# Kernel optimization log

Hardware: AMD Instinct MI355X
Metric: run time of the kernel (lower is better)

The kernel has to match this reference:

```python
import jax, jax.numpy as jnp
import numpy as np

N_NODES = 10000
N_EDGES = 320000
NUM_NEIGHBORS = 32.0
INV_SQRT3 = 1.0 / np.sqrt(3.0)  # component-normalized CG for 1o x 1o -> 0e


def setup_inputs() -> dict:
    key = jax.random.key(0)
    ks = jax.random.split(key, 16)
    f32 = jnp.float32
    return {
        "node_input": jax.random.normal(ks[0], (N_NODES, 160), f32),   # 64x0e | 32x1o
        "node_attr": jnp.ones((N_NODES, 1), f32),                       # 1x0e
        "edge_attr": jax.random.normal(ks[1], (N_EDGES, 4), f32),       # 1x0e | 1x1o (sph harm)
        "edge_scalar_attr": jax.random.normal(ks[2], (N_EDGES, 8), f32),# radial basis
        "Wsc0": jax.random.normal(ks[3], (64, 64), f32),
        "Wsc1": jax.random.normal(ks[4], (32, 32), f32),
        "Wl1_0": jax.random.normal(ks[5], (64, 64), f32),
        "Wl1_1": jax.random.normal(ks[6], (32, 32), f32),
        "Wfc1": jax.random.normal(ks[7], (8, 64), f32),
        "Wfc2": jax.random.normal(ks[8], (64, 64), f32),
        "Wfc3": jax.random.normal(ks[9], (64, 192), f32),  # -> tp.weight_numel
        "Wl2_s": jax.random.normal(ks[10], (96, 64), f32),
        "Wl2_v": jax.random.normal(ks[11], (96, 32), f32),
        "Wa": jax.random.normal(ks[12], (96, 1), f32),
        "edge_src": jax.random.randint(ks[13], (N_EDGES,), 0, N_NODES),
        "edge_dst": jax.random.randint(ks[14], (N_EDGES,), 0, N_NODES),
    }


def _fctp_scalar_attr(xs, xv, Ws, Wv, a):
    """FullyConnectedTensorProduct(irreps, '0e', irreps) with scalar node attr a.
    xs: [N, mul_s] scalars, xv: [N, mul_v, 3] vectors. Path-normalized by 1/sqrt(fan_in)."""
    out_s = (xs @ Ws) * (a / np.sqrt(xs.shape[1]))[:, None]
    out_v = jnp.einsum('nuc,uw->nwc', xv, Wv) * (a / np.sqrt(xv.shape[1]))[:, None, None]
    return out_s, out_v


def reference(node_input, node_attr, edge_attr, edge_scalar_attr,
              Wsc0, Wsc1, Wl1_0, Wl1_1, Wfc1, Wfc2, Wfc3, Wl2_s, Wl2_v, Wa,
              edge_src, edge_dst):
    N = node_input.shape[0]
    a = node_attr[:, 0]                              # [N] scalar attr
    xs = node_input[:, :64]                          # [N,64]  64x0e
    xv = node_input[:, 64:].reshape(N, 32, 3)        # [N,32,3] 32x1o

    # self connection: FCTp(input, attr, output)
    sc_s, sc_v = _fctp_scalar_attr(xs, xv, Wsc0, Wsc1, a)
    # lin1: FCTp(input, attr, input)
    f_s, f_v = _fctp_scalar_attr(xs, xv, Wl1_0, Wl1_1, a)

    # radial MLP -> tensor-product weights [E, 192]
    h = jax.nn.gelu(edge_scalar_attr @ Wfc1 / np.sqrt(8.0))
    h = jax.nn.gelu(h @ Wfc2 / np.sqrt(64.0))
    w = h @ Wfc3 / np.sqrt(64.0)
    w0, w1, w2, w3 = w[:, :64], w[:, 64:128], w[:, 128:160], w[:, 160:192]

    # gather source node features per edge
    gs = f_s[edge_src]                               # [E,64]
    gv = f_v[edge_src]                               # [E,32,3]
    y0 = edge_attr[:, 0]                             # [E]   0e
    y1 = edge_attr[:, 1:4]                           # [E,3] 1o

    # 'uvu' tensor product, irreps_mid (sorted) = 64x0e + 32x0e + 64x1o + 32x1o
    mid0 = w0 * gs * y0[:, None]                                        # 0e x 0e -> 0e
    mid1 = w3 * jnp.einsum('euc,ec->eu', gv, y1) * INV_SQRT3            # 1o x 1o -> 0e
    mid2 = (w1 * gs)[:, :, None] * y1[:, None, :]                       # 0e x 1o -> 1o
    mid3 = w2[:, :, None] * gv * y0[:, None, None]                      # 1o x 0e -> 1o

    # scatter-add to destination nodes, normalized by sqrt(num_neighbors)
    inv = 1.0 / np.sqrt(NUM_NEIGHBORS)
    seg = lambda x: jax.ops.segment_sum(x, edge_dst, num_segments=N) * inv
    ns0, ns1, nv2, nv3 = seg(mid0), seg(mid1), seg(mid2), seg(mid3)

    mid_s = jnp.concatenate([ns0, ns1], axis=1)      # [N,96] scalars of irreps_mid
    mid_v = jnp.concatenate([nv2, nv3], axis=1)      # [N,96,3] vectors of irreps_mid

    # lin2: FCTp(mid, attr, output), fan_in = 96 for both scalar and vector outputs
    out_s = (mid_s @ Wl2_s) * (a / np.sqrt(96.0))[:, None]
    out_v = jnp.einsum('nuc,uw->nwc', mid_v, Wl2_v) * (a / np.sqrt(96.0))[:, None, None]

    # alpha: FCTp(mid, attr, '0e'); self_con output_mask is all ones here
    alpha = (mid_s @ Wa) * (a / np.sqrt(96.0))[:, None]  # [N,1]

    res_s = sc_s + alpha * out_s
    res_v = sc_v + alpha[:, :, None] * out_v
    return jnp.concatenate([res_s, res_v.reshape(N, 96)], axis=1)  # [N,160]
```

## Files before the change

### kernel.cpp

```cpp
#include <hip/hip_runtime.h>

#define N_NODES 10000
#define N_EDGES 320000
#define INV3 0.5773502691896258f

typedef short short8 __attribute__((ext_vector_type(8)));
typedef float f32x4 __attribute__((ext_vector_type(4)));

__device__ __forceinline__ float gelu_f(float x) {
    float x3 = x * x * x;
    float e = __expf(-1.5957691216057308f * (x + 0.044715f * x3));
    return x * __builtin_amdgcn_rcpf(1.0f + e);
}

__device__ __forceinline__ unsigned short f2bf(float f) {
    unsigned u = __float_as_uint(f);
    unsigned r = (u + 0x7FFFu + ((u >> 16) & 1u)) >> 16;
    return (unsigned short)r;
}
__device__ __forceinline__ float bf2f(unsigned short u) {
    return __uint_as_float(((unsigned)u) << 16);
}
__device__ __forceinline__ unsigned cvtpk(float lo, float hi) {
    unsigned r;
    asm("v_cvt_pk_bf16_f32 %0, %1, %2" : "=v"(r) : "v"(lo), "v"(hi));
    return r;
}

__device__ __forceinline__ float rowsum16(float v) {
    v += __int_as_float(__builtin_amdgcn_update_dpp(0, __float_as_int(v), 0x118, 0xf, 0xf, true));
    v += __int_as_float(__builtin_amdgcn_update_dpp(0, __float_as_int(v), 0x114, 0xf, 0xf, true));
    v += __int_as_float(__builtin_amdgcn_update_dpp(0, __float_as_int(v), 0x112, 0xf, 0xf, true));
    v += __int_as_float(__builtin_amdgcn_update_dpp(0, __float_as_int(v), 0x111, 0xf, 0xf, true));
    return v;
}

__global__ __launch_bounds__(256) void pre_kernel(
    const int* __restrict__ edge_dst, int* __restrict__ deg,
    const float* __restrict__ Wfc1, const float* __restrict__ Wfc2,
    const float* __restrict__ Wfc3, uint4* __restrict__ fragbuf,
    const float* __restrict__ node_input, const float* __restrict__ node_attr,
    const float* __restrict__ Wl1_0, const float* __restrict__ Wl1_1,
    unsigned short* __restrict__ f_sb, unsigned short* __restrict__ f_vb,
    int* __restrict__ bcnt)
{
    const int b = blockIdx.x;
    if (b < 1250) {
        int e = b * 256 + threadIdx.x;
        if (e < N_EDGES) atomicAdd(&deg[edge_dst[e]], 1);
        return;
    }
    if (b < 1259) {
        if (b == 1250 && threadIdx.x < 64) bcnt[threadIdx.x] = 0;
        const int tile = (b - 1250) * 4 + (threadIdx.x >> 6);
        if (tile >= 36) return;
        const int l = threadIdx.x & 63;
        const int e = l & 15, g = l >> 4;
        unsigned p[4] = {0u, 0u, 0u, 0u};
        if (tile < 4) {
            if (g == 0) {
                #pragma unroll
                for (int j = 0; j < 8; ++j) {
                    unsigned short bb = f2bf(Wfc1[j * 64 + tile * 16 + e]);
                    p[j >> 1] |= (unsigned)bb << (16 * (j & 1));
                }
            }
        } else if (tile < 12) {
            int t2 = tile - 4; int mt = t2 >> 1, kt = t2 & 1;
            #pragma unroll
            for (int j = 0; j < 8; ++j) {
                unsigned short bb = f2bf(Wfc2[(kt * 32 + g * 8 + j) * 64 + mt * 16 + e]);
                p[j >> 1] |= (unsigned)bb << (16 * (j & 1));
            }
        } else {
            int t3 = tile - 12; int mt3 = t3 >> 1, kt = t3 & 1;
            #pragma unroll
            for (int j = 0; j < 8; ++j) {
                unsigned short bb = f2bf(Wfc3[(kt * 32 + g * 8 + j) * 192 + mt3 * 16 + e]);
                p[j >> 1] |= (unsigned)bb << (16 * (j & 1));
            }
        }
        uint4 v; v.x = p[0]; v.y = p[1]; v.z = p[2]; v.w = p[3];
        fragbuf[tile * 64 + l] = v;
        return;
    }
    const int wid = threadIdx.x >> 6;
    const int t = threadIdx.x & 63;
    const int n = (b - 1259) * 4 + wid;
    __shared__ float x[4][160];
    const float* row = node_input + (size_t)n * 160;
    for (int i = t; i < 160; i += 64) x[wid][i] = row[i];
    const float a = node_attr[n];

    float acc = 0.f;
    for (int k = 0; k < 64; ++k) acc += x[wid][k] * Wl1_0[k * 64 + t];
    f_sb[(size_t)n * 64 + t] = f2bf(acc * (a * 0.125f));

    const float sv = a * 0.17677669529663687f;
    for (int o = t; o < 96; o += 64) {
        int w = o / 3, c = o - w * 3;
        float av = 0.f;
        for (int u = 0; u < 32; ++u) av += x[wid][64 + u * 3 + c] * Wl1_1[u * 32 + w];
        f_vb[(size_t)n * 96 + o] = f2bf(av * sv);
    }
}

__global__ __launch_bounds__(256) void alloc_kernel(const int* __restrict__ deg,
                                                    int* __restrict__ gctr,
                                                    int* __restrict__ done,
                                                    int* __restrict__ rowptr,
                                                    int* __restrict__ cursor,
                                                    int* __restrict__ bcnt,
                                                    int* __restrict__ bcur) {
    const int tid = threadIdx.x;
    const int n = blockIdx.x * 256 + tid;
    const int d = (n < N_NODES) ? deg[n] : 0;

    __shared__ int part[256];
    __shared__ int blockbase;
    __shared__ int lb[64];
    __shared__ int islast;
    part[tid] = d;
    if (tid < 64) lb[tid] = 0;
    __syncthreads();
    for (int o = 1; o < 256; o <<= 1) {
        int v = (tid >= o) ? part[tid - o] : 0;
        __syncthreads();
        part[tid] += v;
        __syncthreads();
    }
    if (tid == 255) blockbase = atomicAdd(gctr, part[255]);
    __syncthreads();
    const int base = blockbase + part[tid] - d;
    if (n < N_NODES) {
        rowptr[n] = base;
        cursor[n] = base;
        int nt = (d + 15) >> 4; if (nt > 63) nt = 63;
        atomicAdd(&lb[nt], 1);
    }
    __syncthreads();
    if (tid < 64 && lb[tid]) {
        int ack = atomicAdd(&bcnt[tid], lb[tid]);
        asm volatile("" :: "v"(ack));
    }
    __syncthreads();
    if (tid == 0) islast = (atomicAdd(done, 1) == (int)gridDim.x - 1);
    __syncthreads();
    if (islast && tid == 0) {
        int run = 0;
        for (int i = 63; i >= 0; --i) { bcur[i] = run; run += atomicAdd(&bcnt[i], 0); }
    }
}

__global__ __launch_bounds__(256) void post_kernel(const int* __restrict__ dst,
                                                   const int* __restrict__ deg,
                                                   int* __restrict__ cursor,
                                                   int* __restrict__ elist,
                                                   int* __restrict__ bcur,
                                                   int* __restrict__ nodeperm) {
    const int b = blockIdx.x;
    if (b < 40) {
        const int tid = threadIdx.x;
        const int n = b * 256 + tid;
        __shared__ int lcnt[64], lbase[64];
        if (tid < 64) lcnt[tid] = 0;
        __syncthreads();
        int nt = 63, my = 0;
        if (n < N_NODES) {
            int d = deg[n];
            nt = (d + 15) >> 4; if (nt > 63) nt = 63;
            my = atomicAdd(&lcnt[nt], 1);
        }
        __syncthreads();
        if (tid < 64 && lcnt[tid]) lbase[tid] = atomicAdd(&bcur[tid], lcnt[tid]);
        __syncthreads();
        if (n < N_NODES) nodeperm[lbase[nt] + my] = n;
        return;
    }
    int e = (b - 40) * 256 + threadIdx.x;
    if (e < N_EDGES) {
        int p = atomicAdd(&cursor[dst[e]], 1);
        elist[p] = e;
    }
}

#define L3CHUNK(mt3_, d_) { \
    short8 a0_ = ((short8*)wfrag)[(12 + (mt3_) * 2 + 0) * 64 + l]; \
    short8 a1_ = ((short8*)wfrag)[(12 + (mt3_) * 2 + 1) * 64 + l]; \
    d_[0] = 0.f; d_[1] = 0.f; d_[2] = 0.f; d_[3] = 0.f; \
    d_ = __builtin_amdgcn_mfma_f32_16x16x32_bf16(a0_, bh0, d_, 0, 0, 0); \
    d_ = __builtin_amdgcn_mfma_f32_16x16x32_bf16(a1_, bh1, d_, 0, 0, 0); }

__global__ __launch_bounds__(256) __attribute__((amdgpu_waves_per_eu(2, 4)))
void fused_kernel(
    const float* __restrict__ edge_attr,
    const float* __restrict__ esa,
    const unsigned short* __restrict__ f_sb,
    const unsigned short* __restrict__ f_vb,
    const int* __restrict__ edge_src,
    const int* __restrict__ elist,
    const int* __restrict__ rowptr,
    const int* __restrict__ deg,
    const int* __restrict__ nodeperm,
    const float4* __restrict__ fragbuf,
    const float* __restrict__ node_input,
    const float* __restrict__ node_attr,
    const float* __restrict__ Wsc0,
    const float* __restrict__ Wsc1,
    const float* __restrict__ Wl2_s,
    const float* __restrict__ Wl2_v,
    const float* __restrict__ Wa,
    float* __restrict__ out)
{
    __shared__ __align__(16) char wfrag[36864];
    __shared__ __align__(16) char albuf[2 * 4096];
    __shared__ __align__(16) float xld[2][160];

    const int tid = threadIdx.x;
    const int l = tid & 63;
    const int wid = tid >> 6;
    const int q = wid & 1;
    const int ns = wid >> 1;

    {
        float4* w = (float4*)wfrag;
        #pragma unroll
        for (int i = 0; i < 9; ++i) w[tid + 256 * i] = fragbuf[tid + 256 * i];
    }

    const int n0 = nodeperm[blockIdx.x * 2 + 0];
    const int n1 = nodeperm[blockIdx.x * 2 + 1];
    const int n = ns ? n1 : n0;
    const int dn0 = deg[n0], dn1 = deg[n1];
    const int ntmax = ((dn0 > dn1 ? dn0 : dn1) + 15) >> 4;
    const int p0 = rowptr[n];
    const int p1 = p0 + (ns ? dn1 : dn0);
    const int p0c = p0 < N_EDGES ? p0 : N_EDGES - 1;

    if (q == 0)
        for (int i = l; i < 160; i += 64) xld[ns][i] = node_input[(size_t)n * 160 + i];

    __syncthreads();

    const int er = l & 15, gr = l >> 4;
    const int swz = (er & 7) << 4;
    char* h1b = albuf + ns * 4096;
    char* h2b = h1b + 2048;

    float acc0[2][4];
    float acc1[4];
    float acc2[2][4][3];
    float acc3[4][3];
    #pragma unroll
    for (int jj = 0; jj < 2; ++jj)
        #pragma unroll
        for (int r = 0; r < 4; ++r) {
            acc0[jj][r] = 0.f;
            acc2[jj][r][0] = 0.f; acc2[jj][r][1] = 0.f; acc2[jj][r][2] = 0.f;
        }
    #pragma unroll
    for (int r = 0; r < 4; ++r) {
        acc1[r] = 0.f;
        acc3[r][0] = 0.f; acc3[r][1] = 0.f; acc3[r][2] = 0.f;
    }

    float4 ea = {0.f, 0.f, 0.f, 0.f};
    int src = 0;
    uint4 bxu = {0u, 0u, 0u, 0u};
    if (ntmax > 0) {
        const int ci = p0 + er;
        const bool cv = ci < p1;
        const int ec = elist[cv ? ci : p0c];
        ea = ((const float4*)edge_attr)[ec];
        src = edge_src[ec];
        if (l < 16 && cv) {
            float4 xa = ((const float4*)esa)[(size_t)ec * 2 + 0];
            float4 xb = ((const float4*)esa)[(size_t)ec * 2 + 1];
            bxu.x = cvtpk(xa.x, xa.y);
            bxu.y = cvtpk(xa.z, xa.w);
            bxu.z = cvtpk(xb.x, xb.y);
            bxu.w = cvtpk(xb.z, xb.w);
        }
    }

    #pragma unroll 1
    for (int it = 0; it < ntmax; ++it) {
        const float y0 = ea.x, y1a = ea.y, y1b = ea.z, y1c = ea.w;
        union { uint4 u; short8 s; } bxc; bxc.u = bxu;
        const short8 bx = bxc.s;
        const int csrc = src;

        ushort4 gsu0 = *(const ushort4*)(f_sb + (size_t)csrc * 64 + (q * 2 + 0) * 16 + gr * 4);
        ushort4 gsu1 = *(const ushort4*)(f_sb + (size_t)csrc * 64 + (q * 2 + 1) * 16 + gr * 4);
        const unsigned short* gvp = f_vb + (size_t)csrc * 96 + (size_t)(q * 16 + gr * 4) * 3;
        ushort4 ga = *(const ushort4*)(gvp + 0);
        ushort4 gb = *(const ushort4*)(gvp + 4);
        ushort4 gc = *(const ushort4*)(gvp + 8);

        {
            const int np = p0 + (it + 1) * 16;
            const bool nv = (np + er) < p1;
            const int nec = elist[nv ? np + er : p0c];
            float4 nea = ((const float4*)edge_attr)[nec];
            int nsrc = edge_src[nec];
            uint4 nbxu = {0u, 0u, 0u, 0u};
            if (l < 16 && nv) {
                float4 xa = ((const float4*)esa)[(size_t)nec * 2 + 0];
                float4 xb = ((const float4*)esa)[(size_t)nec * 2 + 1];
                nbxu.x = cvtpk(xa.x, xa.y);
                nbxu.y = cvtpk(xa.z, xa.w);
                nbxu.z = cvtpk(xb.x, xb.y);
                nbxu.w = cvtpk(xb.z, xb.w);
            }
            ea = nea; src = nsrc; bxu = nbxu;
        }

        #pragma unroll
        for (int j = 0; j < 2; ++j) {
            const int mt = q * 2 + j;
            short8 aw = ((short8*)wfrag)[mt * 64 + l];
            f32x4 c = {0.f, 0.f, 0.f, 0.f};
            c = __builtin_amdgcn_mfma_f32_16x16x32_bf16(aw, bx, c, 0, 0, 0);
            unsigned pa = cvtpk(gelu_f(c[0] * 0.35355339059327373f),
                                gelu_f(c[1] * 0.35355339059327373f));
            unsigned pb = cvtpk(gelu_f(c[2] * 0.35355339059327373f),
                                gelu_f(c[3] * 0.35355339059327373f));
            uint2 pv; pv.x = pa; pv.y = pb;
            *(uint2*)(h1b + ((er * 128 + mt * 32 + gr * 8) ^ swz)) = pv;
        }
        __syncthreads();
        {
            short8 b0 = *(short8*)(h1b + ((er * 128 + 0  + gr * 16) ^ swz));
            short8 b1 = *(short8*)(h1b + ((er * 128 + 64 + gr * 16) ^ swz));
            #pragma unroll
            for (int j = 0; j < 2; ++j) {
                const int mt = q * 2 + j;
                short8 w2a = ((short8*)(wfrag + 4096))[(2 * mt + 0) * 64 + l];
                short8 w2b = ((short8*)(wfrag + 4096))[(2 * mt + 1) * 64 + l];
                f32x4 c = {0.f, 0.f, 0.f, 0.f};
                c = __builtin_amdgcn_mfma_f32_16x16x32_bf16(w2a, b0, c, 0, 0, 0);
                c = __builtin_amdgcn_mfma_f32_16x16x32_bf16(w2b, b1, c, 0, 0, 0);
                unsigned pa = cvtpk(gelu_f(c[0] * 0.125f), gelu_f(c[1] * 0.125f));
                unsigned pb = cvtpk(gelu_f(c[2] * 0.125f), gelu_f(c[3] * 0.125f));
                uint2 pv; pv.x = pa; pv.y = pb;
                *(uint2*)(h2b + ((er * 128 + mt * 32 + gr * 8) ^ swz)) = pv;
            }
        }
        __syncthreads();
        short8 bh0 = *(short8*)(h2b + ((er * 128 + 0  + gr * 16) ^ swz));
        short8 bh1 = *(short8*)(h2b + ((er * 128 + 64 + gr * 16) ^ swz));

        #pragma unroll
        for (int jj = 0; jj < 2; ++jj) {
            const int jg = q * 2 + jj;
            ushort4 gsu = jj ? gsu1 : gsu0;
            f32x4 gs4 = {bf2f(gsu.x), bf2f(gsu.y), bf2f(gsu.z), bf2f(gsu.w)};
            f32x4 dA; L3CHUNK(jg, dA);
            f32x4 dB; L3CHUNK(jg + 4, dB);
            #pragma unroll
            for (int r = 0; r < 4; ++r) {
                acc0[jj][r] += 0.125f * dA[r] * gs4[r] * y0;
                float t_ = 0.125f * dB[r] * gs4[r];
                acc2[jj][r][0] += t_ * y1a;
                acc2[jj][r][1] += t_ * y1b;
                acc2[jj][r][2] += t_ * y1c;
            }
        }
        {
            const int jv = q;
            float gv[12] = {bf2f(ga.x), bf2f(ga.y), bf2f(ga.z), bf2f(ga.w),
                            bf2f(gb.x), bf2f(gb.y), bf2f(gb.z), bf2f(gb.w),
                            bf2f(gc.x), bf2f(gc.y), bf2f(gc.z), bf2f(gc.w)};
            f32x4 dC; L3CHUNK(8 + jv, dC);
            f32x4 dD; L3CHUNK(10 + jv, dD);
            #pragma unroll
            for (int r = 0; r < 4; ++r) {
                float w2v = 0.125f * dC[r] * y0;
                acc3[r][0] += w2v * gv[r * 3 + 0];
                acc3[r][1] += w2v * gv[r * 3 + 1];
                acc3[r][2] += w2v * gv[r * 3 + 2];
                float dot = gv[r * 3 + 0] * y1a + gv[r * 3 + 1] * y1b + gv[r * 3 + 2] * y1c;
                acc1[r] += 0.125f * dD[r] * dot * INV3;
            }
        }
    }

    #pragma unroll
    for (int jj = 0; jj < 2; ++jj)
        #pragma unroll
        for (int r = 0; r < 4; ++r) {
            acc0[jj][r] = rowsum16(acc0[jj][r]);
            acc2[jj][r][0] = rowsum16(acc2[jj][r][0]);
            acc2[jj][r][1] = rowsum16(acc2[jj][r][1]);
            acc2[jj][r][2] = rowsum16(acc2[jj][r][2]);
        }
    #pragma unroll
    for (int r = 0; r < 4; ++r) {
        acc1[r] = rowsum16(acc1[r]);
        acc3[r][0] = rowsum16(acc3[r][0]);
        acc3[r][1] = rowsum16(acc3[r][1]);
        acc3[r][2] = rowsum16(acc3[r][2]);
    }

    __syncthreads();

    float* m = (float*)(albuf + ns * 4096);
    const float iN = 0.17677669529663687f;
    if (er == 15) {
        #pragma unroll
        for (int jj = 0; jj < 2; ++jj) {
            const int jg = q * 2 + jj;
            f32x4 v;
            v[0] = acc0[jj][0] * iN; v[1] = acc0[jj][1] * iN;
            v[2] = acc0[jj][2] * iN; v[3] = acc0[jj][3] * iN;
            *(f32x4*)(m + jg * 16 + gr * 4) = v;
        }
        {
            const int jv = q;
            f32x4 v;
            v[0] = acc1[0] * iN; v[1] = acc1[1] * iN;
            v[2] = acc1[2] * iN; v[3] = acc1[3] * iN;
            *(f32x4*)(m + 64 + jv * 16 + gr * 4) = v;
        }
        #pragma unroll
        for (int jj = 0; jj < 2; ++jj) {
            const int jg = q * 2 + jj;
            float t[12];
            #pragma unroll
            for (int r = 0; r < 4; ++r) {
                t[r * 3 + 0] = acc2[jj][r][0] * iN;
                t[r * 3 + 1] = acc2[jj][r][1] * iN;
                t[r * 3 + 2] = acc2[jj][r][2] * iN;
            }
            float* b = m + 96 + (jg * 16 + gr * 4) * 3;
            *(f32x4*)(b + 0) = (f32x4){t[0], t[1], t[2], t[3]};
            *(f32x4*)(b + 4) = (f32x4){t[4], t[5], t[6], t[7]};
            *(f32x4*)(b + 8) = (f32x4){t[8], t[9], t[10], t[11]};
        }
        {
            const int jv = q;
            float t[12];
            #pragma unroll
            for (int r = 0; r < 4; ++r) {
                t[r * 3 + 0] = acc3[r][0] * iN;
                t[r * 3 + 1] = acc3[r][1] * iN;
                t[r * 3 + 2] = acc3[r][2] * iN;
            }
            float* b = m + 288 + (jv * 16 + gr * 4) * 3;
            *(f32x4*)(b + 0) = (f32x4){t[0], t[1], t[2], t[3]};
            *(f32x4*)(b + 4) = (f32x4){t[4], t[5], t[6], t[7]};
            *(f32x4*)(b + 8) = (f32x4){t[8], t[9], t[10], t[11]};
        }
    }

    __syncthreads();

    const float a = node_attr[n];
    const float* x = xld[ns];
    const float s96 = a * 0.10206207261596575f;

    float alpha = 0.f;
    for (int i = 0; i < 96; ++i) alpha += m[i] * Wa[i];
    alpha *= s96;

    if (q == 0) {
        float outs = 0.f;
        for (int i = 0; i < 96; ++i) outs += m[i] * Wl2_s[i * 64 + l];
        outs *= s96;
        float scs = 0.f;
        for (int k = 0; k < 64; ++k) scs += x[k] * Wsc0[k * 64 + l];
        scs *= a * 0.125f;
        out[(size_t)n * 160 + l] = scs + alpha * outs;
    } else {
        const float sv = a * 0.17677669529663687f;
        for (int o = l; o < 96; o += 64) {
            int w = o / 3, c = o - w * 3;
            float ov = 0.f;
            for (int u = 0; u < 64; ++u) ov += m[96 + u * 3 + c] * Wl2_v[u * 32 + w];
            for (int u = 0; u < 32; ++u) ov += m[288 + u * 3 + c] * Wl2_v[(64 + u) * 32 + w];
            ov *= s96;
            float scv = 0.f;
            for (int u = 0; u < 32; ++u) scv += x[64 + u * 3 + c] * Wsc1[u * 32 + w];
            scv *= sv;
            out[(size_t)n * 160 + 64 + o] = scv + alpha * ov;
        }
    }
}

extern "C" void kernel_launch(void* const* d_in, const int* in_sizes, int n_in,
                              void* d_out, int out_size, void* d_ws, size_t ws_size,
                              hipStream_t stream) {
    const float* node_input = (const float*)d_in[0];
    const float* node_attr  = (const float*)d_in[1];
    const float* edge_attr  = (const float*)d_in[2];
    const float* esa        = (const float*)d_in[3];
    const float* Wsc0       = (const float*)d_in[4];
    const float* Wsc1       = (const float*)d_in[5];
    const float* Wl1_0      = (const float*)d_in[6];
    const float* Wl1_1      = (const float*)d_in[7];
    const float* Wfc1       = (const float*)d_in[8];
    const float* Wfc2       = (const float*)d_in[9];
    const float* Wfc3       = (const float*)d_in[10];
    const float* Wl2_s      = (const float*)d_in[11];
    const float* Wl2_v      = (const float*)d_in[12];
    const float* Wa         = (const float*)d_in[13];
    const int* edge_src     = (const int*)d_in[14];
    const int* edge_dst     = (const int*)d_in[15];
    float* out = (float*)d_out;

    float* ws  = (float*)d_ws;
    unsigned short* f_sb = (unsigned short*)ws;
    unsigned short* f_vb = (unsigned short*)(ws + 320000);
    uint4* fragbuf = (uint4*)(ws + 1600000);
    int* ibuf     = (int*)(ws + 1609216);
    int* deg      = ibuf;
    int* gctr     = ibuf + 10000;
    int* done     = ibuf + 10001;
    int* rowptr   = ibuf + 10016;
    int* cursor   = ibuf + 20032;
    int* elist    = ibuf + 30080;
    int* bcnt     = ibuf + 350080;
    int* bcur     = ibuf + 350144;
    int* nodeperm = ibuf + 350208;

    hipMemsetAsync(deg, 0, (size_t)(N_NODES + 2) * sizeof(int), stream);

    pre_kernel<<<3759, 256, 0, stream>>>(edge_dst, deg, Wfc1, Wfc2, Wfc3, fragbuf,
                                         node_input, node_attr, Wl1_0, Wl1_1, f_sb, f_vb, bcnt);
    alloc_kernel<<<(N_NODES + 255) / 256, 256, 0, stream>>>(deg, gctr, done, rowptr,
                                                            cursor, bcnt, bcur);
    post_kernel<<<40 + (N_EDGES + 255) / 256, 256, 0, stream>>>(edge_dst, deg, cursor,
                                                                elist, bcur, nodeperm);

    fused_kernel<<<N_NODES / 2, 256, 0, stream>>>(edge_attr, esa, f_sb, f_vb,
                                                  edge_src, elist, rowptr, deg, nodeperm,
                                                  (const float4*)fragbuf,
                                                  node_input, node_attr,
                                                  Wsc0, Wsc1, Wl2_s, Wl2_v, Wa,
                                                  out);
}
```

Baseline: 177.2 us.

## Process three nodes per block and two edge tiles per iteration

The fused kernel now runs 384 threads per block and handles three destination nodes instead of two. Each loop iteration now processes two 16-edge tiles with duplicated MFMA and GELU streams, which halves the number of block barriers per edge and adds more independent work to hide latency. The 0.125 scale of the last layer moves into the precomputed bf16 node features, so the inner loop does fewer multiplies. In exchange it uses more registers and LDS per block, and it takes the tile count from the first node only, which relies on the node permutation putting the highest-degree node first in each block.

```diff
diff --git a/kernel.cpp b/kernel.cpp
--- a/kernel.cpp
+++ b/kernel.cpp
@@ -94,14 +94,14 @@
 
     float acc = 0.f;
     for (int k = 0; k < 64; ++k) acc += x[wid][k] * Wl1_0[k * 64 + t];
-    f_sb[(size_t)n * 64 + t] = f2bf(acc * (a * 0.125f));
+    f_sb[(size_t)n * 64 + t] = f2bf(acc * (a * 0.125f) * 0.125f);
 
     const float sv = a * 0.17677669529663687f;
     for (int o = t; o < 96; o += 64) {
         int w = o / 3, c = o - w * 3;
         float av = 0.f;
         for (int u = 0; u < 32; ++u) av += x[wid][64 + u * 3 + c] * Wl1_1[u * 32 + w];
-        f_vb[(size_t)n * 96 + o] = f2bf(av * sv);
+        f_vb[(size_t)n * 96 + o] = f2bf(av * sv * 0.125f);
     }
 }
 
@@ -184,14 +184,66 @@
     }
 }
 
-#define L3CHUNK(mt3_, d_) { \
+#define MFMA16(a_, b_, c_) __builtin_amdgcn_mfma_f32_16x16x32_bf16(a_, b_, c_, 0, 0, 0)
+
+#define L3CHUNK2(mt3_, bh0_, bh1_, d_) { \
     short8 a0_ = ((short8*)wfrag)[(12 + (mt3_) * 2 + 0) * 64 + l]; \
     short8 a1_ = ((short8*)wfrag)[(12 + (mt3_) * 2 + 1) * 64 + l]; \
     d_[0] = 0.f; d_[1] = 0.f; d_[2] = 0.f; d_[3] = 0.f; \
-    d_ = __builtin_amdgcn_mfma_f32_16x16x32_bf16(a0_, bh0, d_, 0, 0, 0); \
-    d_ = __builtin_amdgcn_mfma_f32_16x16x32_bf16(a1_, bh1, d_, 0, 0, 0); }
-
-__global__ __launch_bounds__(256) __attribute__((amdgpu_waves_per_eu(2, 4)))
+    d_ = MFMA16(a0_, bh0_, d_); \
+    d_ = MFMA16(a1_, bh1_, d_); }
+
+#define TPSUB(bh0_, bh1_, gsu0_, gsu1_, ga_, gb_, gc_, y0_, y1a_, y1b_, y1c_) { \
+    _Pragma("unroll") \
+    for (int jj = 0; jj < 2; ++jj) { \
+        const int jg = q * 2 + jj; \
+        ushort4 gsu = jj ? gsu1_ : gsu0_; \
+        f32x4 gs4 = {bf2f(gsu.x), bf2f(gsu.y), bf2f(gsu.z), bf2f(gsu.w)}; \
+        f32x4 dA; L3CHUNK2(jg, bh0_, bh1_, dA); \
+        f32x4 dB; L3CHUNK2(jg + 4, bh0_, bh1_, dB); \
+        _Pragma("unroll") \
+        for (int r = 0; r < 4; ++r) { \
+            acc0[jj][r] += dA[r] * gs4[r] * y0_; \
+            float t_ = dB[r] * gs4[r]; \
+            acc2[jj][r][0] += t_ * y1a_; \
+            acc2[jj][r][1] += t_ * y1b_; \
+            acc2[jj][r][2] += t_ * y1c_; \
+        } \
+    } \
+    { \
+        float gv[12] = {bf2f(ga_.x), bf2f(ga_.y), bf2f(ga_.z), bf2f(ga_.w), \
+                        bf2f(gb_.x), bf2f(gb_.y), bf2f(gb_.z), bf2f(gb_.w), \
+                        bf2f(gc_.x), bf2f(gc_.y), bf2f(gc_.z), bf2f(gc_.w)}; \
+        f32x4 dC; L3CHUNK2(8 + q, bh0_, bh1_, dC); \
+        f32x4 dD; L3CHUNK2(10 + q, bh0_, bh1_, dD); \
+        _Pragma("unroll") \
+        for (int r = 0; r < 4; ++r) { \
+            float w2v = dC[r] * y0_; \
+            acc3[r][0] += w2v * gv[r * 3 + 0]; \
+            acc3[r][1] += w2v * gv[r * 3 + 1]; \
+            acc3[r][2] += w2v * gv[r * 3 + 2]; \
+            float dot = gv[r * 3 + 0] * y1a_ + gv[r * 3 + 1] * y1b_ + gv[r * 3 + 2] * y1c_; \
+            acc1[r] += dD[r] * dot * INV3; \
+        } \
+    } }
+
+#define LOADSTATE(s_, ea_, src_, bxu_) { \
+    const int ci_ = p0 + (s_) * 16 + er; \
+    const bool cv_ = ci_ < p1; \
+    const int ec_ = elist[cv_ ? ci_ : p0c]; \
+    ea_ = ((const float4*)edge_attr)[ec_]; \
+    src_ = edge_src[ec_]; \
+    bxu_.x = 0u; bxu_.y = 0u; bxu_.z = 0u; bxu_.w = 0u; \
+    if (l < 16 && cv_) { \
+        float4 xa_ = ((const float4*)esa)[(size_t)ec_ * 2 + 0]; \
+        float4 xb_ = ((const float4*)esa)[(size_t)ec_ * 2 + 1]; \
+        bxu_.x = cvtpk(xa_.x, xa_.y); \
+        bxu_.y = cvtpk(xa_.z, xa_.w); \
+        bxu_.z = cvtpk(xb_.x, xb_.y); \
+        bxu_.w = cvtpk(xb_.z, xb_.w); \
+    } }
+
+__global__ __launch_bounds__(384) __attribute__((amdgpu_waves_per_eu(2, 4)))
 void fused_kernel(
     const float* __restrict__ edge_attr,
     const float* __restrict__ esa,
@@ -213,8 +265,8 @@
     float* __restrict__ out)
 {
     __shared__ __align__(16) char wfrag[36864];
-    __shared__ __align__(16) char albuf[2 * 4096];
-    __shared__ __align__(16) float xld[2][160];
+    __shared__ __align__(16) char albuf[3 * 8192];
+    __shared__ __align__(16) float xld[3][160];
 
     const int tid = threadIdx.x;
     const int l = tid & 63;
@@ -225,27 +277,30 @@
     {
         float4* w = (float4*)wfrag;
         #pragma unroll
-        for (int i = 0; i < 9; ++i) w[tid + 256 * i] = fragbuf[tid + 256 * i];
-    }
-
-    const int n0 = nodeperm[blockIdx.x * 2 + 0];
-    const int n1 = nodeperm[blockIdx.x * 2 + 1];
-    const int n = ns ? n1 : n0;
-    const int dn0 = deg[n0], dn1 = deg[n1];
-    const int ntmax = ((dn0 > dn1 ? dn0 : dn1) + 15) >> 4;
+        for (int i = 0; i < 6; ++i) w[tid + 384 * i] = fragbuf[tid + 384 * i];
+    }
+
+    const int nidx = blockIdx.x * 3 + ns;
+    const bool nvalid = nidx < N_NODES;
+    const int n = nodeperm[nvalid ? nidx : N_NODES - 1];
+    const int dmy = nvalid ? deg[n] : 0;
+    const int n0 = nodeperm[blockIdx.x * 3];
+    const int ntmax = (deg[n0] + 15) >> 4;
     const int p0 = rowptr[n];
-    const int p1 = p0 + (ns ? dn1 : dn0);
+    const int p1 = p0 + dmy;
     const int p0c = p0 < N_EDGES ? p0 : N_EDGES - 1;
 
-    if (q == 0)
+    if (q == 0 && nvalid)
         for (int i = l; i < 160; i += 64) xld[ns][i] = node_input[(size_t)n * 160 + i];
 
     __syncthreads();
 
     const int er = l & 15, gr = l >> 4;
     const int swz = (er & 7) << 4;
-    char* h1b = albuf + ns * 4096;
-    char* h2b = h1b + 2048;
+    char* h1A = albuf + ns * 8192;
+    char* h1B = h1A + 2048;
+    char* h2A = h1A + 4096;
+    char* h2B = h1A + 6144;
 
     float acc0[2][4];
     float acc1[4];
@@ -264,125 +319,90 @@
         acc3[r][0] = 0.f; acc3[r][1] = 0.f; acc3[r][2] = 0.f;
     }
 
-    float4 ea = {0.f, 0.f, 0.f, 0.f};
-    int src = 0;
-    uint4 bxu = {0u, 0u, 0u, 0u};
+    float4 eaA = {0.f, 0.f, 0.f, 0.f}, eaB = {0.f, 0.f, 0.f, 0.f};
+    int srcA = 0, srcB = 0;
+    uint4 bxuA = {0u, 0u, 0u, 0u}, bxuB = {0u, 0u, 0u, 0u};
     if (ntmax > 0) {
-        const int ci = p0 + er;
-        const bool cv = ci < p1;
-        const int ec = elist[cv ? ci : p0c];
-        ea = ((const float4*)edge_attr)[ec];
-        src = edge_src[ec];
-        if (l < 16 && cv) {
-            float4 xa = ((const float4*)esa)[(size_t)ec * 2 + 0];
-            float4 xb = ((const float4*)esa)[(size_t)ec * 2 + 1];
-            bxu.x = cvtpk(xa.x, xa.y);
-            bxu.y = cvtpk(xa.z, xa.w);
-            bxu.z = cvtpk(xb.x, xb.y);
-            bxu.w = cvtpk(xb.z, xb.w);
-        }
+        LOADSTATE(0, eaA, srcA, bxuA);
+        LOADSTATE(1, eaB, srcB, bxuB);
     }
 
     #pragma unroll 1
-    for (int it = 0; it < ntmax; ++it) {
-        const float y0 = ea.x, y1a = ea.y, y1b = ea.z, y1c = ea.w;
-        union { uint4 u; short8 s; } bxc; bxc.u = bxu;
-        const short8 bx = bxc.s;
-        const int csrc = src;
-
-        ushort4 gsu0 = *(const ushort4*)(f_sb + (size_t)csrc * 64 + (q * 2 + 0) * 16 + gr * 4);
-        ushort4 gsu1 = *(const ushort4*)(f_sb + (size_t)csrc * 64 + (q * 2 + 1) * 16 + gr * 4);
-        const unsigned short* gvp = f_vb + (size_t)csrc * 96 + (size_t)(q * 16 + gr * 4) * 3;
-        ushort4 ga = *(const ushort4*)(gvp + 0);
-        ushort4 gb = *(const ushort4*)(gvp + 4);
-        ushort4 gc = *(const ushort4*)(gvp + 8);
-
-        {
-            const int np = p0 + (it + 1) * 16;
-            const bool nv = (np + er) < p1;
-            const int nec = elist[nv ? np + er : p0c];
-            float4 nea = ((const float4*)edge_attr)[nec];
-            int nsrc = edge_src[nec];
-            uint4 nbxu = {0u, 0u, 0u, 0u};
-            if (l < 16 && nv) {
-                float4 xa = ((const float4*)esa)[(size_t)nec * 2 + 0];
-                float4 xb = ((const float4*)esa)[(size_t)nec * 2 + 1];
-                nbxu.x = cvtpk(xa.x, xa.y);
-                nbxu.y = cvtpk(xa.z, xa.w);
-                nbxu.z = cvtpk(xb.x, xb.y);
-                nbxu.w = cvtpk(xb.z, xb.w);
-            }
-            ea = nea; src = nsrc; bxu = nbxu;
-        }
+    for (int it = 0; it < ntmax; it += 2) {
+        const float y0A = eaA.x, y1aA = eaA.y, y1bA = eaA.z, y1cA = eaA.w;
+        const float y0B = eaB.x, y1aB = eaB.y, y1bB = eaB.z, y1cB = eaB.w;
+        union { uint4 u; short8 s; } bc0; bc0.u = bxuA; const short8 bxA = bc0.s;
+        union { uint4 u; short8 s; } bc1; bc1.u = bxuB; const short8 bxB = bc1.s;
+        const int csrcA = srcA, csrcB = srcB;
+
+        ushort4 gsu0A = *(const ushort4*)(f_sb + (size_t)csrcA * 64 + (q * 2 + 0) * 16 + gr * 4);
+        ushort4 gsu1A = *(const ushort4*)(f_sb + (size_t)csrcA * 64 + (q * 2 + 1) * 16 + gr * 4);
+        const unsigned short* gvpA = f_vb + (size_t)csrcA * 96 + (size_t)(q * 16 + gr * 4) * 3;
+        ushort4 gaA = *(const ushort4*)(gvpA + 0);
+        ushort4 gbA = *(const ushort4*)(gvpA + 4);
+        ushort4 gcA = *(const ushort4*)(gvpA + 8);
+        ushort4 gsu0B = *(const ushort4*)(f_sb + (size_t)csrcB * 64 + (q * 2 + 0) * 16 + gr * 4);
+        ushort4 gsu1B = *(const ushort4*)(f_sb + (size_t)csrcB * 64 + (q * 2 + 1) * 16 + gr * 4);
+        const unsigned short* gvpB = f_vb + (size_t)csrcB * 96 + (size_t)(q * 16 + gr * 4) * 3;
+        ushort4 gaB = *(const ushort4*)(gvpB + 0);
+        ushort4 gbB = *(const ushort4*)(gvpB + 4);
+        ushort4 gcB = *(const ushort4*)(gvpB + 8);
+
+        LOADSTATE(it + 2, eaA, srcA, bxuA);
+        LOADSTATE(it + 3, eaB, srcB, bxuB);
 
         #pragma unroll
         for (int j = 0; j < 2; ++j) {
             const int mt = q * 2 + j;
             short8 aw = ((short8*)wfrag)[mt * 64 + l];
-            f32x4 c = {0.f, 0.f, 0.f, 0.f};
-            c = __builtin_amdgcn_mfma_f32_16x16x32_bf16(aw, bx, c, 0, 0, 0);
-            unsigned pa = cvtpk(gelu_f(c[0] * 0.35355339059327373f),
-                                gelu_f(c[1] * 0.35355339059327373f));
-            unsigned pb = cvtpk(gelu_f(c[2] * 0.35355339059327373f),
-                                gelu_f(c[3] * 0.35355339059327373f));
-            uint2 pv; pv.x = pa; pv.y = pb;
-            *(uint2*)(h1b + ((er * 128 + mt * 32 + gr * 8) ^ swz)) = pv;
+            f32x4 cA = {0.f, 0.f, 0.f, 0.f};
+            cA = MFMA16(aw, bxA, cA);
+            f32x4 cB = {0.f, 0.f, 0.f, 0.f};
+            cB = MFMA16(aw, bxB, cB);
+            uint2 pvA;
+            pvA.x = cvtpk(gelu_f(cA[0] * 0.35355339059327373f), gelu_f(cA[1] * 0.35355339059327373f));
+            pvA.y = cvtpk(gelu_f(cA[2] * 0.35355339059327373f), gelu_f(cA[3] * 0.35355339059327373f));
+            *(uint2*)(h1A + ((er * 128 + mt * 32 + gr * 8) ^ swz)) = pvA;
+            uint2 pvB;
+            pvB.x = cvtpk(gelu_f(cB[0] * 0.35355339059327373f), gelu_f(cB[1] * 0.35355339059327373f));
+            pvB.y = cvtpk(gelu_f(cB[2] * 0.35355339059327373f), gelu_f(cB[3] * 0.35355339059327373f));
+            *(uint2*)(h1B + ((er * 128 + mt * 32 + gr * 8) ^ swz)) = pvB;
         }
         __syncthreads();
         {
-            short8 b0 = *(short8*)(h1b + ((er * 128 + 0  + gr * 16) ^ swz));
-            short8 b1 = *(short8*)(h1b + ((er * 128 + 64 + gr * 16) ^ swz));
+            short8 b0A = *(short8*)(h1A + ((er * 128 + 0  + gr * 16) ^ swz));
+            short8 b1A = *(short8*)(h1A + ((er * 128 + 64 + gr * 16) ^ swz));
+            short8 b0B = *(short8*)(h1B + ((er * 128 + 0  + gr * 16) ^ swz));
+            short8 b1B = *(short8*)(h1B + ((er * 128 + 64 + gr * 16) ^ swz));
             #pragma unroll
             for (int j = 0; j < 2; ++j) {
                 const int mt = q * 2 + j;
                 short8 w2a = ((short8*)(wfrag + 4096))[(2 * mt + 0) * 64 + l];
                 short8 w2b = ((short8*)(wfrag + 4096))[(2 * mt + 1) * 64 + l];
-                f32x4 c = {0.f, 0.f, 0.f, 0.f};
-                c = __builtin_amdgcn_mfma_f32_16x16x32_bf16(w2a, b0, c, 0, 0, 0);
-                c = __builtin_amdgcn_mfma_f32_16x16x32_bf16(w2b, b1, c, 0, 0, 0);
-                unsigned pa = cvtpk(gelu_f(c[0] * 0.125f), gelu_f(c[1] * 0.125f));
-                unsigned pb = cvtpk(gelu_f(c[2] * 0.125f), gelu_f(c[3] * 0.125f));
-                uint2 pv; pv.x = pa; pv.y = pb;
-                *(uint2*)(h2b + ((er * 128 + mt * 32 + gr * 8) ^ swz)) = pv;
+                f32x4 cA = {0.f, 0.f, 0.f, 0.f};
+                cA = MFMA16(w2a, b0A, cA);
+                cA = MFMA16(w2b, b1A, cA);
+                f32x4 cB = {0.f, 0.f, 0.f, 0.f};
+                cB = MFMA16(w2a, b0B, cB);
+                cB = MFMA16(w2b, b1B, cB);
+                uint2 pvA;
+                pvA.x = cvtpk(gelu_f(cA[0] * 0.125f), gelu_f(cA[1] * 0.125f));
+                pvA.y = cvtpk(gelu_f(cA[2] * 0.125f), gelu_f(cA[3] * 0.125f));
+                *(uint2*)(h2A + ((er * 128 + mt * 32 + gr * 8) ^ swz)) = pvA;
+                uint2 pvB;
+                pvB.x = cvtpk(gelu_f(cB[0] * 0.125f), gelu_f(cB[1] * 0.125f));
+                pvB.y = cvtpk(gelu_f(cB[2] * 0.125f), gelu_f(cB[3] * 0.125f));
+                *(uint2*)(h2B + ((er * 128 + mt * 32 + gr * 8) ^ swz)) = pvB;
             }
         }
         __syncthreads();
-        short8 bh0 = *(short8*)(h2b + ((er * 128 + 0  + gr * 16) ^ swz));
-        short8 bh1 = *(short8*)(h2b + ((er * 128 + 64 + gr * 16) ^ swz));
-
-        #pragma unroll
-        for (int jj = 0; jj < 2; ++jj) {
-            const int jg = q * 2 + jj;
-            ushort4 gsu = jj ? gsu1 : gsu0;
-            f32x4 gs4 = {bf2f(gsu.x), bf2f(gsu.y), bf2f(gsu.z), bf2f(gsu.w)};
-            f32x4 dA; L3CHUNK(jg, dA);
-            f32x4 dB; L3CHUNK(jg + 4, dB);
-            #pragma unroll
-            for (int r = 0; r < 4; ++r) {
-                acc0[jj][r] += 0.125f * dA[r] * gs4[r] * y0;
-                float t_ = 0.125f * dB[r] * gs4[r];
-                acc2[jj][r][0] += t_ * y1a;
-                acc2[jj][r][1] += t_ * y1b;
-                acc2[jj][r][2] += t_ * y1c;
-            }
-        }
-        {
-            const int jv = q;
-            float gv[12] = {bf2f(ga.x), bf2f(ga.y), bf2f(ga.z), bf2f(ga.w),
-                            bf2f(gb.x), bf2f(gb.y), bf2f(gb.z), bf2f(gb.w),
-                            bf2f(gc.x), bf2f(gc.y), bf2f(gc.z), bf2f(gc.w)};
-            f32x4 dC; L3CHUNK(8 + jv, dC);
-            f32x4 dD; L3CHUNK(10 + jv, dD);
-            #pragma unroll
-            for (int r = 0; r < 4; ++r) {
-                float w2v = 0.125f * dC[r] * y0;
-                acc3[r][0] += w2v * gv[r * 3 + 0];
-                acc3[r][1] += w2v * gv[r * 3 + 1];
-                acc3[r][2] += w2v * gv[r * 3 + 2];
-                float dot = gv[r * 3 + 0] * y1a + gv[r * 3 + 1] * y1b + gv[r * 3 + 2] * y1c;
-                acc1[r] += 0.125f * dD[r] * dot * INV3;
-            }
-        }
+        short8 bh0A = *(short8*)(h2A + ((er * 128 + 0  + gr * 16) ^ swz));
+        short8 bh1A = *(short8*)(h2A + ((er * 128 + 64 + gr * 16) ^ swz));
+        short8 bh0B = *(short8*)(h2B + ((er * 128 + 0  + gr * 16) ^ swz));
+        short8 bh1B = *(short8*)(h2B + ((er * 128 + 64 + gr * 16) ^ swz));
+
+        TPSUB(bh0A, bh1A, gsu0A, gsu1A, gaA, gbA, gcA, y0A, y1aA, y1bA, y1cA);
+        TPSUB(bh0B, bh1B, gsu0B, gsu1B, gaB, gbB, gcB, y0B, y1aB, y1bB, y1cB);
     }
 
     #pragma unroll
@@ -404,7 +424,7 @@
 
     __syncthreads();
 
-    float* m = (float*)(albuf + ns * 4096);
+    float* m = (float*)(albuf + ns * 8192);
     const float iN = 0.17677669529663687f;
     if (er == 15) {
         #pragma unroll
@@ -416,11 +436,10 @@
             *(f32x4*)(m + jg * 16 + gr * 4) = v;
         }
         {
-            const int jv = q;
             f32x4 v;
             v[0] = acc1[0] * iN; v[1] = acc1[1] * iN;
             v[2] = acc1[2] * iN; v[3] = acc1[3] * iN;
-            *(f32x4*)(m + 64 + jv * 16 + gr * 4) = v;
+            *(f32x4*)(m + 64 + q * 16 + gr * 4) = v;
         }
         #pragma unroll
         for (int jj = 0; jj < 2; ++jj) {
@@ -438,7 +457,6 @@
             *(f32x4*)(b + 8) = (f32x4){t[8], t[9], t[10], t[11]};
         }
         {
-            const int jv = q;
             float t[12];
             #pragma unroll
             for (int r = 0; r < 4; ++r) {
@@ -446,7 +464,7 @@
                 t[r * 3 + 1] = acc3[r][1] * iN;
                 t[r * 3 + 2] = acc3[r][2] * iN;
             }
-            float* b = m + 288 + (jv * 16 + gr * 4) * 3;
+            float* b = m + 288 + (q * 16 + gr * 4) * 3;
             *(f32x4*)(b + 0) = (f32x4){t[0], t[1], t[2], t[3]};
             *(f32x4*)(b + 4) = (f32x4){t[4], t[5], t[6], t[7]};
             *(f32x4*)(b + 8) = (f32x4){t[8], t[9], t[10], t[11]};
@@ -454,6 +472,8 @@
     }
 
     __syncthreads();
+
+    if (!nvalid) return;
 
     const float a = node_attr[n];
     const float* x = xld[ns];
@@ -532,10 +552,10 @@
     post_kernel<<<40 + (N_EDGES + 255) / 256, 256, 0, stream>>>(edge_dst, deg, cursor,
                                                                 elist, bcur, nodeperm);
 
-    fused_kernel<<<N_NODES / 2, 256, 0, stream>>>(edge_attr, esa, f_sb, f_vb,
-                                                  edge_src, elist, rowptr, deg, nodeperm,
-                                                  (const float4*)fragbuf,
-                                                  node_input, node_attr,
-                                                  Wsc0, Wsc1, Wl2_s, Wl2_v, Wa,
-                                                  out);
-}
+    fused_kernel<<<(N_NODES + 2) / 3, 384, 0, stream>>>(edge_attr, esa, f_sb, f_vb,
+                                                        edge_src, elist, rowptr, deg, nodeperm,
+                                                        (const float4*)fragbuf,
+                                                        node_input, node_attr,
+                                                        Wsc0, Wsc1, Wl2_s, Wl2_v, Wa,
+                                                        out);
+}
```

Result: slower. 268.5 us (+51.5%).
